# Optimization experiments

Measured on AMD Instinct MI355X. Metric: run time of the kernel, lower is better.

The kernel has to match this reference:

```python
import jax, jax.numpy as jnp
import numpy as np

HEADS = 6
WIN = 7
SHIFT = 3
NEG = -100.0


def _rel_index():
    # Swin relative position index, [49, 49] int
    coords = np.stack(np.meshgrid(np.arange(WIN), np.arange(WIN), indexing='ij')).reshape(2, -1)
    rel = (coords[:, :, None] - coords[:, None, :]).transpose(1, 2, 0)
    rel[:, :, 0] += WIN - 1
    rel[:, :, 1] += WIN - 1
    rel[:, :, 0] *= 2 * WIN - 1
    return rel.sum(-1)


def _shift_mask(H, W):
    # additive shift mask per window, [num_windows, 49, 49]
    img = np.zeros([H, W])
    slices = (slice(0, -WIN), slice(-WIN, -SHIFT), slice(-SHIFT, None))
    cnt = 0
    for h in slices:
        for w in slices:
            img[h, w] = cnt
            cnt += 1
    mw = img.reshape(H // WIN, WIN, W // WIN, WIN).transpose(0, 2, 1, 3).reshape(-1, WIN * WIN)
    diff = mw[:, None, :] - mw[:, :, None]
    return np.where(diff != 0, NEG, 0.0).astype(np.float32)


def setup_inputs() -> dict:
    key = jax.random.key(0)
    ks = jax.random.split(key, 6)
    B, H, W, C = 64, 56, 56, 192
    return {
        'x': jax.random.normal(ks[0], (B, H, W, C), jnp.float32),
        'qkv_w': jax.random.normal(ks[1], (C, 3 * C), jnp.float32) * 0.02,
        'qkv_b': jax.random.normal(ks[2], (3 * C,), jnp.float32) * 0.02,
        'rel_table': jax.random.normal(ks[3], ((2 * WIN - 1) ** 2, HEADS), jnp.float32) * 0.02,
        'proj_w': jax.random.normal(ks[4], (C, C), jnp.float32) * 0.02,
        'proj_b': jax.random.normal(ks[5], (C,), jnp.float32) * 0.02,
    }


def reference(x, qkv_w, qkv_b, rel_table, proj_w, proj_b):
    B, H, W, C = x.shape
    hd = C // HEADS
    scale = hd ** -0.5
    mask = jnp.asarray(_shift_mask(H, W))            # [nW, N, N]
    idx = _rel_index().reshape(-1)                   # static numpy [N*N]

    # cyclic shift + window partition
    xs = jnp.roll(x, (-SHIFT, -SHIFT), (1, 2))
    xw = xs.reshape(B, H // WIN, WIN, W // WIN, WIN, C)
    xw = xw.transpose(0, 1, 3, 2, 4, 5).reshape(-1, WIN * WIN, C)  # [Bn, N, C]
    Bn, N, _ = xw.shape

    qkv = (xw @ qkv_w + qkv_b).reshape(Bn, N, 3, HEADS, hd).transpose(2, 0, 3, 1, 4)
    q, k, v = qkv[0] * scale, qkv[1], qkv[2]         # [Bn, h, N, hd]

    attn = jax.nn.softmax(jnp.einsum('bhnd,bhmd->bhnm', q, k), axis=-1)

    # NOTE: original module adds relative bias and shift mask AFTER softmax
    bias = rel_table[idx].reshape(N, N, HEADS).transpose(2, 0, 1)  # [h, N, N]
    attn = attn + bias[None]
    nW = mask.shape[0]
    attn = (attn.reshape(Bn // nW, nW, HEADS, N, N) + mask[None, :, None]).reshape(Bn, HEADS, N, N)

    out = jnp.einsum('bhnm,bhmd->bhnd', attn, v).transpose(0, 2, 1, 3).reshape(Bn, N, C)
    out = out @ proj_w + proj_b

    # window reverse + un-shift
    out = out.reshape(B, H // WIN, W // WIN, WIN, WIN, C)
    out = out.transpose(0, 1, 3, 2, 4, 5).reshape(B, H, W, C)
    return jnp.roll(out, (SHIFT, SHIFT), (1, 2))
```

## Files before the change

kernel.cpp:

```cpp
#include <hip/hip_runtime.h>
#include <hip/hip_bf16.h>

typedef __attribute__((ext_vector_type(8))) short bf16x8_t;
typedef __attribute__((ext_vector_type(4))) float f32x4_t;

#define MFMA16 __builtin_amdgcn_mfma_f32_16x16x32_bf16

__device__ __forceinline__ unsigned short f2bf(float f) {
    return __builtin_bit_cast(unsigned short, __float2bfloat16(f));
}
__device__ __forceinline__ int cvt_pk_bf16(float lo, float hi) {
    int r;
    asm("v_cvt_pk_bf16_f32 %0, %1, %2" : "=v"(r) : "v"(lo), "v"(hi));
    return r;
}

__device__ __forceinline__ void group_barrier(int* cnt, int target, int ln) {
    asm volatile("s_waitcnt lgkmcnt(0)" ::: "memory");
    if (ln == 0)
        __hip_atomic_fetch_add(cnt, 1, __ATOMIC_RELEASE, __HIP_MEMORY_SCOPE_WORKGROUP);
    while (__hip_atomic_load(cnt, __ATOMIC_ACQUIRE, __HIP_MEMORY_SCOPE_WORKGROUP) < target)
        __builtin_amdgcn_s_sleep(1);
    __builtin_amdgcn_sched_barrier(0);
}

#define GRP_STRIDE 49152
#define ROWOFF_OFF 98304
#define BAR_OFF    98816
#define SMEM_BYTES 98832

__device__ __forceinline__ int qk_byte(int row, int d) {
    return row * 64 + ((((d >> 3) ^ ((row >> 1) & 3)) << 4) | ((d & 7) << 1));
}
__device__ __forceinline__ int vt_byte(int d, int tok) {
    return d * 128 + ((((tok >> 3) ^ (d & 7)) << 4) | ((tok & 7) << 1));
}

__global__ void prep_weights(const float* __restrict__ qkv_w, const float* __restrict__ proj_w,
                             unsigned short* __restrict__ wqkvT, unsigned short* __restrict__ wprojT)
{
    int i = blockIdx.x * 256 + threadIdx.x;
    if (i < 576 * 192) {
        int n = i / 192, k = i - n * 192;
        wqkvT[i] = f2bf(qkv_w[k * 576 + n]);
    }
    if (i < 192 * 192) {
        int n = i / 192, k = i - n * 192;
        wprojT[i] = f2bf(proj_w[k * 192 + n]);
    }
}

__global__ void prep_bias(const float* __restrict__ rel_table, float* __restrict__ biasT)
{
    int i = blockIdx.x * 256 + threadIdx.x;
    if (i >= 4 * 6 * 16 * 64) return;
    int ln  = i & 63;
    int f   = (i >> 6) & 15;
    int h   = (i >> 10) % 6;
    int wt  = i / 6144;
    int l15 = ln & 15, lg = ln >> 4;
    int mk  = f >> 2, nq = f & 3;
    int qt  = nq * 16 + l15;
    bool bh = (wt & 2) != 0, bw = (wt & 1) != 0;
    float4 o = {0.f, 0.f, 0.f, 0.f};
    float* po = (float*)&o;
    int iq = qt / 7, jq = qt - iq * 7;
    int regq = (bh ? ((iq < 4) ? 3 : 6) : 0) + (bw ? ((jq < 4) ? 1 : 2) : 0);
    for (int r = 0; r < 4; ++r) {
        int kt = mk * 16 + lg * 4 + r;
        if (kt < 49 && qt < 49) {
            int ik = kt / 7, jk = kt - ik * 7;
            int idx = (iq - ik + 6) * 13 + (jq - jk + 6);
            int regk = (bh ? ((ik < 4) ? 3 : 6) : 0) + (bw ? ((jk < 4) ? 1 : 2) : 0);
            po[r] = rel_table[idx * 6 + h] + ((regk != regq) ? -100.0f : 0.0f);
        }
    }
    ((float4*)biasT)[i] = o;
}

__global__ __launch_bounds__(768, 3)
void swin_fused(const float* __restrict__ x,
                const float* __restrict__ qkv_b,
                const float* __restrict__ proj_b,
                const unsigned short* __restrict__ wqkvT,
                const unsigned short* __restrict__ wprojT,
                const float* __restrict__ biasT,
                float* __restrict__ out)
{
    __shared__ unsigned char smem[SMEM_BYTES];

    const int tid = threadIdx.x;
    const int wv  = tid >> 6;
    const int g   = (wv >= 6) ? 1 : 0;
    const int h   = wv - 6 * g;
    const int ln  = tid & 63;
    const int l15 = ln & 15;
    const int lg  = ln >> 4;
    const int tg  = tid - g * 384;

    const int bw  = blockIdx.x * 2 + g;
    const int b   = bw >> 6;
    const int win = bw & 63;
    const int wh  = win >> 3;
    const int ww  = win & 7;
    const int wt  = ((wh == 7) ? 2 : 0) | ((ww == 7) ? 1 : 0);

    const unsigned gbase = g * GRP_STRIDE;
    const unsigned hbase = gbase + h * 8192;
    int* rowOff = (int*)(smem + ROWOFF_OFF + g * 256);
    int* bar    = (int*)(smem + BAR_OFF) + g;
    const f32x4_t zero4 = {0.f, 0.f, 0.f, 0.f};

    if (tid < 2) ((int*)(smem + BAR_OFF))[tid] = 0;
    __syncthreads();

#pragma unroll
    for (int it = 0; it < 8; ++it) {
        int idx = tg + it * 384;
        int n   = idx / 48;
        int c4  = idx - n * 48;
        int2* dst = (int2*)(smem + gbase + n * 400 + c4 * 8);
        if (n < 49) {
            int i = n / 7, j = n - i * 7;
            int sh = wh * 7 + i + 3; if (sh >= 56) sh -= 56;
            int sw = ww * 7 + j + 3; if (sw >= 56) sw -= 56;
            int ro = ((b * 56 + sh) * 56 + sw) * 192;
            if (c4 == 0) rowOff[n] = ro;
            const float4* src = (const float4*)(x + ro + c4 * 4);
            float4 v = *src;
            int2 p;
            p.x = cvt_pk_bf16(v.x, v.y);
            p.y = cvt_pk_bf16(v.z, v.w);
            *dst = p;
        } else {
            *dst = make_int2(0, 0);
        }
    }
    group_barrier(bar, 6, ln);

    f32x4_t accq[4][6];
#pragma unroll
    for (int mt = 0; mt < 4; ++mt)
#pragma unroll
        for (int nt = 0; nt < 6; ++nt) accq[mt][nt] = zero4;
#pragma unroll
    for (int ks = 0; ks < 6; ++ks) {
        bf16x8_t af[4];
#pragma unroll
        for (int mt = 0; mt < 4; ++mt)
            af[mt] = *(const bf16x8_t*)(smem + gbase + (mt * 16 + l15) * 400 + (ks * 32 + lg * 8) * 2);
        bf16x8_t bfv[6];
#pragma unroll
        for (int nt = 0; nt < 6; ++nt)
            bfv[nt] = *(const bf16x8_t*)(wqkvT + ((nt >> 1) * 192 + h * 32 + (nt & 1) * 16 + l15) * 192 + ks * 32 + lg * 8);
        __builtin_amdgcn_s_setprio(1);
#pragma unroll
        for (int nt = 0; nt < 6; ++nt)
#pragma unroll
            for (int mt = 0; mt < 4; ++mt)
                accq[mt][nt] = MFMA16(af[mt], bfv[nt], accq[mt][nt], 0, 0, 0);
        __builtin_amdgcn_s_setprio(0);
    }
    int vbf[4][2][2];
#pragma unroll
    for (int nv = 0; nv < 2; ++nv) {
        float bb = qkv_b[384 + h * 32 + nv * 16 + l15];
#pragma unroll
        for (int mt = 0; mt < 4; ++mt) {
            vbf[mt][nv][0] = cvt_pk_bf16(accq[mt][4 + nv][0] + bb, accq[mt][4 + nv][1] + bb);
            vbf[mt][nv][1] = cvt_pk_bf16(accq[mt][4 + nv][2] + bb, accq[mt][4 + nv][3] + bb);
        }
    }
    group_barrier(bar, 12, ln);

#pragma unroll
    for (int nt = 0; nt < 4; ++nt) {
        int part = nt >> 1;
        int d    = (nt & 1) * 16 + l15;
        float bb = qkv_b[part * 192 + h * 32 + d];
        unsigned base = hbase + part * 4096;
#pragma unroll
        for (int mt = 0; mt < 4; ++mt)
#pragma unroll
            for (int r = 0; r < 4; ++r) {
                int row = mt * 16 + lg * 4 + r;
                *(unsigned short*)(smem + base + qk_byte(row, d)) = f2bf(accq[mt][nt][r] + bb);
            }
    }
    __builtin_amdgcn_sched_barrier(0);

    f32x4_t s[4][4];
    {
        bf16x8_t kf[4], qf[4];
#pragma unroll
        for (int mk = 0; mk < 4; ++mk) {
            int row = mk * 16 + l15;
            kf[mk] = *(const bf16x8_t*)(smem + hbase + 4096 + row * 64 + ((lg ^ ((row >> 1) & 3)) << 4));
        }
#pragma unroll
        for (int nq = 0; nq < 4; ++nq) {
            int row = nq * 16 + l15;
            qf[nq] = *(const bf16x8_t*)(smem + hbase + row * 64 + ((lg ^ ((row >> 1) & 3)) << 4));
        }
        __builtin_amdgcn_s_setprio(1);
#pragma unroll
        for (int mk = 0; mk < 4; ++mk)
#pragma unroll
            for (int nq = 0; nq < 4; ++nq)
                s[mk][nq] = MFMA16(kf[mk], qf[nq], zero4, 0, 0, 0);
        __builtin_amdgcn_s_setprio(0);
    }
    __builtin_amdgcn_sched_barrier(0);

#pragma unroll
    for (int nv = 0; nv < 2; ++nv) {
        int d = nv * 16 + l15;
#pragma unroll
        for (int mt = 0; mt < 4; ++mt) {
            int tok = mt * 16 + lg * 4;
            *(int2*)(smem + hbase + vt_byte(d, tok)) = make_int2(vbf[mt][nv][0], vbf[mt][nv][1]);
        }
    }

    float4 bv4[4][4];
    {
        const float4* bp = (const float4*)biasT + (wt * 6 + h) * 16 * 64 + ln;
#pragma unroll
        for (int mk = 0; mk < 4; ++mk)
#pragma unroll
            for (int nq = 0; nq < 4; ++nq)
                bv4[mk][nq] = bp[(mk * 4 + nq) * 64];
    }

    const float C = 0.17677669529663687f * 1.4426950408889634f;
#pragma unroll
    for (int nq = 0; nq < 4; ++nq) {
        float sum = 0.f;
#pragma unroll
        for (int mk = 0; mk < 4; ++mk)
#pragma unroll
            for (int r = 0; r < 4; ++r) {
                int kt = mk * 16 + lg * 4 + r;
                float e = (kt < 49) ? __builtin_amdgcn_exp2f(C * s[mk][nq][r]) : 0.0f;
                s[mk][nq][r] = e;
                sum += e;
            }
        sum += __shfl_xor(sum, 16);
        sum += __shfl_xor(sum, 32);
        float inv = __builtin_amdgcn_rcpf(sum);
#pragma unroll
        for (int mk = 0; mk < 4; ++mk)
#pragma unroll
            for (int r = 0; r < 4; ++r) s[mk][nq][r] *= inv;
    }

#pragma unroll
    for (int mk = 0; mk < 4; ++mk)
#pragma unroll
        for (int nq = 0; nq < 4; ++nq) {
            s[mk][nq][0] += bv4[mk][nq].x;
            s[mk][nq][1] += bv4[mk][nq].y;
            s[mk][nq][2] += bv4[mk][nq].z;
            s[mk][nq][3] += bv4[mk][nq].w;
        }

    int w[4][4][2];
#pragma unroll
    for (int mk = 0; mk < 4; ++mk)
#pragma unroll
        for (int nq = 0; nq < 4; ++nq) {
            w[mk][nq][0] = cvt_pk_bf16(s[mk][nq][0], s[mk][nq][1]);
            w[mk][nq][1] = cvt_pk_bf16(s[mk][nq][2], s[mk][nq][3]);
        }

    f32x4_t o[2][4];
#pragma unroll
    for (int md = 0; md < 2; ++md)
#pragma unroll
        for (int nq = 0; nq < 4; ++nq) o[md][nq] = zero4;

    const unsigned Abase = hbase + 4096;
#pragma unroll
    for (int ks = 0; ks < 2; ++ks) {
#pragma unroll
        for (int mh = 0; mh < 2; ++mh) {
            int mk = ks * 2 + mh;
            int d  = mh * 16 + lg * 4;
#pragma unroll
            for (int nq = 0; nq < 4; ++nq) {
                int qt = nq * 16 + l15;
                *(int2*)(smem + Abase + qk_byte(qt, d)) = make_int2(w[mk][nq][0], w[mk][nq][1]);
            }
        }
        __builtin_amdgcn_sched_barrier(0);
        bf16x8_t vf[2], bfr[4];
#pragma unroll
        for (int md = 0; md < 2; ++md) {
            int d = md * 16 + l15;
            vf[md] = *(const bf16x8_t*)(smem + hbase + d * 128 + (((ks * 4 + lg) ^ (d & 7)) << 4));
        }
#pragma unroll
        for (int nq = 0; nq < 4; ++nq) {
            int qt = nq * 16 + l15;
            bfr[nq] = *(const bf16x8_t*)(smem + Abase + qt * 64 + ((lg ^ ((qt >> 1) & 3)) << 4));
        }
        __builtin_amdgcn_s_setprio(1);
#pragma unroll
        for (int nq = 0; nq < 4; ++nq)
#pragma unroll
            for (int md = 0; md < 2; ++md)
                o[md][nq] = MFMA16(vf[md], bfr[nq], o[md][nq], 0, 0, 0);
        __builtin_amdgcn_s_setprio(0);
        __builtin_amdgcn_sched_barrier(0);
    }
    group_barrier(bar, 18, ln);

#pragma unroll
    for (int md = 0; md < 2; ++md)
#pragma unroll
        for (int nq = 0; nq < 4; ++nq) {
            int qt = nq * 16 + l15;
            int ch = h * 32 + md * 16 + lg * 4;
            int d0 = cvt_pk_bf16(o[md][nq][0], o[md][nq][1]);
            int d1 = cvt_pk_bf16(o[md][nq][2], o[md][nq][3]);
            *(int2*)(smem + gbase + qt * 400 + ch * 2) = make_int2(d0, d1);
        }
    group_barrier(bar, 24, ln);

    f32x4_t y[4][2];
#pragma unroll
    for (int mt = 0; mt < 4; ++mt) { y[mt][0] = zero4; y[mt][1] = zero4; }
#pragma unroll
    for (int ks = 0; ks < 6; ++ks) {
        bf16x8_t aa[4], bb[2];
#pragma unroll
        for (int mt = 0; mt < 4; ++mt)
            aa[mt] = *(const bf16x8_t*)(smem + gbase + (mt * 16 + l15) * 400 + (ks * 32 + lg * 8) * 2);
#pragma unroll
        for (int nt = 0; nt < 2; ++nt)
            bb[nt] = *(const bf16x8_t*)(wprojT + (h * 32 + nt * 16 + l15) * 192 + ks * 32 + lg * 8);
        __builtin_amdgcn_s_setprio(1);
#pragma unroll
        for (int mt = 0; mt < 4; ++mt)
#pragma unroll
            for (int nt = 0; nt < 2; ++nt)
                y[mt][nt] = MFMA16(aa[mt], bb[nt], y[mt][nt], 0, 0, 0);
        __builtin_amdgcn_s_setprio(0);
    }
    float pb0 = proj_b[h * 32 + l15];
    float pb1 = proj_b[h * 32 + 16 + l15];
#pragma unroll
    for (int mt = 0; mt < 4; ++mt)
#pragma unroll
        for (int r = 0; r < 4; ++r) {
            int row = mt * 16 + lg * 4 + r;
            if (row < 49) {
                int ro = rowOff[row];
                out[ro + h * 32 + l15]      = y[mt][0][r] + pb0;
                out[ro + h * 32 + 16 + l15] = y[mt][1][r] + pb1;
            }
        }
}

extern "C" void kernel_launch(void* const* d_in, const int* in_sizes, int n_in,
                              void* d_out, int out_size, void* d_ws, size_t ws_size,
                              hipStream_t stream) {
    const float* x         = (const float*)d_in[0];
    const float* qkv_w     = (const float*)d_in[1];
    const float* qkv_b     = (const float*)d_in[2];
    const float* rel_table = (const float*)d_in[3];
    const float* proj_w    = (const float*)d_in[4];
    const float* proj_b    = (const float*)d_in[5];
    float* out = (float*)d_out;

    unsigned short* wqkvT  = (unsigned short*)d_ws;
    unsigned short* wprojT = wqkvT + 576 * 192;
    float* biasT = (float*)((char*)d_ws + 294912);

    prep_weights<<<576, 256, 0, stream>>>(qkv_w, proj_w, wqkvT, wprojT);
    prep_bias<<<96, 256, 0, stream>>>(rel_table, biasT);
    swin_fused<<<2048, 768, 0, stream>>>(x, qkv_b, proj_b, wqkvT, wprojT, biasT, out);
}
```

Before: 232.1 us.

## Use one window per block with hardware barriers instead of group spin barriers

```diff
diff --git a/kernel.cpp b/kernel.cpp
--- a/kernel.cpp
+++ b/kernel.cpp
@@ -15,19 +15,8 @@
     return r;
 }
 
-__device__ __forceinline__ void group_barrier(int* cnt, int target, int ln) {
-    asm volatile("s_waitcnt lgkmcnt(0)" ::: "memory");
-    if (ln == 0)
-        __hip_atomic_fetch_add(cnt, 1, __ATOMIC_RELEASE, __HIP_MEMORY_SCOPE_WORKGROUP);
-    while (__hip_atomic_load(cnt, __ATOMIC_ACQUIRE, __HIP_MEMORY_SCOPE_WORKGROUP) < target)
-        __builtin_amdgcn_s_sleep(1);
-    __builtin_amdgcn_sched_barrier(0);
-}
-
-#define GRP_STRIDE 49152
-#define ROWOFF_OFF 98304
-#define BAR_OFF    98816
-#define SMEM_BYTES 98832
+#define ROWOFF_OFF 49152
+#define SMEM_BYTES 49408
 
 __device__ __forceinline__ int qk_byte(int row, int d) {
     return row * 64 + ((((d >> 3) ^ ((row >> 1) & 3)) << 4) | ((d & 7) << 1));
@@ -78,7 +67,7 @@
     ((float4*)biasT)[i] = o;
 }
 
-__global__ __launch_bounds__(768, 3)
+__global__ __launch_bounds__(384, 4)
 void swin_fused(const float* __restrict__ x,
                 const float* __restrict__ qkv_b,
                 const float* __restrict__ proj_b,
@@ -90,36 +79,28 @@
     __shared__ unsigned char smem[SMEM_BYTES];
 
     const int tid = threadIdx.x;
-    const int wv  = tid >> 6;
-    const int g   = (wv >= 6) ? 1 : 0;
-    const int h   = wv - 6 * g;
+    const int h   = tid >> 6;
     const int ln  = tid & 63;
     const int l15 = ln & 15;
     const int lg  = ln >> 4;
-    const int tg  = tid - g * 384;
-
-    const int bw  = blockIdx.x * 2 + g;
+
+    const int bw  = blockIdx.x;
     const int b   = bw >> 6;
     const int win = bw & 63;
     const int wh  = win >> 3;
     const int ww  = win & 7;
     const int wt  = ((wh == 7) ? 2 : 0) | ((ww == 7) ? 1 : 0);
 
-    const unsigned gbase = g * GRP_STRIDE;
-    const unsigned hbase = gbase + h * 8192;
-    int* rowOff = (int*)(smem + ROWOFF_OFF + g * 256);
-    int* bar    = (int*)(smem + BAR_OFF) + g;
+    const unsigned hbase = h * 8192;
+    int* rowOff = (int*)(smem + ROWOFF_OFF);
     const f32x4_t zero4 = {0.f, 0.f, 0.f, 0.f};
 
-    if (tid < 2) ((int*)(smem + BAR_OFF))[tid] = 0;
-    __syncthreads();
-
 #pragma unroll
     for (int it = 0; it < 8; ++it) {
-        int idx = tg + it * 384;
+        int idx = tid + it * 384;
         int n   = idx / 48;
         int c4  = idx - n * 48;
-        int2* dst = (int2*)(smem + gbase + n * 400 + c4 * 8);
+        int2* dst = (int2*)(smem + n * 400 + c4 * 8);
         if (n < 49) {
             int i = n / 7, j = n - i * 7;
             int sh = wh * 7 + i + 3; if (sh >= 56) sh -= 56;
@@ -136,7 +117,7 @@
             *dst = make_int2(0, 0);
         }
     }
-    group_barrier(bar, 6, ln);
+    __syncthreads();
 
     f32x4_t accq[4][6];
 #pragma unroll
@@ -148,7 +129,7 @@
         bf16x8_t af[4];
 #pragma unroll
         for (int mt = 0; mt < 4; ++mt)
-            af[mt] = *(const bf16x8_t*)(smem + gbase + (mt * 16 + l15) * 400 + (ks * 32 + lg * 8) * 2);
+            af[mt] = *(const bf16x8_t*)(smem + (mt * 16 + l15) * 400 + (ks * 32 + lg * 8) * 2);
         bf16x8_t bfv[6];
 #pragma unroll
         for (int nt = 0; nt < 6; ++nt)
@@ -171,7 +152,7 @@
             vbf[mt][nv][1] = cvt_pk_bf16(accq[mt][4 + nv][2] + bb, accq[mt][4 + nv][3] + bb);
         }
     }
-    group_barrier(bar, 12, ln);
+    __syncthreads();
 
 #pragma unroll
     for (int nt = 0; nt < 4; ++nt) {
@@ -313,7 +294,7 @@
         __builtin_amdgcn_s_setprio(0);
         __builtin_amdgcn_sched_barrier(0);
     }
-    group_barrier(bar, 18, ln);
+    __syncthreads();
 
 #pragma unroll
     for (int md = 0; md < 2; ++md)
@@ -323,9 +304,9 @@
             int ch = h * 32 + md * 16 + lg * 4;
             int d0 = cvt_pk_bf16(o[md][nq][0], o[md][nq][1]);
             int d1 = cvt_pk_bf16(o[md][nq][2], o[md][nq][3]);
-            *(int2*)(smem + gbase + qt * 400 + ch * 2) = make_int2(d0, d1);
-        }
-    group_barrier(bar, 24, ln);
+            *(int2*)(smem + qt * 400 + ch * 2) = make_int2(d0, d1);
+        }
+    __syncthreads();
 
     f32x4_t y[4][2];
 #pragma unroll
@@ -335,7 +316,7 @@
         bf16x8_t aa[4], bb[2];
 #pragma unroll
         for (int mt = 0; mt < 4; ++mt)
-            aa[mt] = *(const bf16x8_t*)(smem + gbase + (mt * 16 + l15) * 400 + (ks * 32 + lg * 8) * 2);
+            aa[mt] = *(const bf16x8_t*)(smem + (mt * 16 + l15) * 400 + (ks * 32 + lg * 8) * 2);
 #pragma unroll
         for (int nt = 0; nt < 2; ++nt)
             bb[nt] = *(const bf16x8_t*)(wprojT + (h * 32 + nt * 16 + l15) * 192 + ks * 32 + lg * 8);
@@ -379,5 +360,5 @@
 
     prep_weights<<<576, 256, 0, stream>>>(qkv_w, proj_w, wqkvT, wprojT);
     prep_bias<<<96, 256, 0, stream>>>(rel_table, biasT);
-    swin_fused<<<2048, 768, 0, stream>>>(x, qkv_b, proj_b, wqkvT, wprojT, biasT, out);
-}
+    swin_fused<<<4096, 384, 0, stream>>>(x, qkv_b, proj_b, wqkvT, wprojT, biasT, out);
+}
```

Result: slower. 489.5 us (+110.9%).

## Feed softmax weights directly to K16 MFMA, skipping the LDS round-trip

Applied to the files above, without the earlier changes.

```diff
diff --git a/kernel.cpp b/kernel.cpp
--- a/kernel.cpp
+++ b/kernel.cpp
@@ -2,9 +2,17 @@
 #include <hip/hip_bf16.h>
 
 typedef __attribute__((ext_vector_type(8))) short bf16x8_t;
+typedef __attribute__((ext_vector_type(4))) short bf16x4_t;
 typedef __attribute__((ext_vector_type(4))) float f32x4_t;
 
 #define MFMA16 __builtin_amdgcn_mfma_f32_16x16x32_bf16
+
+#if __has_builtin(__builtin_amdgcn_mfma_f32_16x16x16bf16_1k)
+#define HAVE_MFMA_K16 1
+#define MFMA16K16 __builtin_amdgcn_mfma_f32_16x16x16bf16_1k
+#else
+#define HAVE_MFMA_K16 0
+#endif
 
 __device__ __forceinline__ unsigned short f2bf(float f) {
     return __builtin_bit_cast(unsigned short, __float2bfloat16(f));
@@ -233,6 +241,7 @@
     }
 
     const float C = 0.17677669529663687f * 1.4426950408889634f;
+    int w[4][4][2];
 #pragma unroll
     for (int nq = 0; nq < 4; ++nq) {
         float sum = 0.f;
@@ -249,36 +258,42 @@
         sum += __shfl_xor(sum, 32);
         float inv = __builtin_amdgcn_rcpf(sum);
 #pragma unroll
-        for (int mk = 0; mk < 4; ++mk)
-#pragma unroll
-            for (int r = 0; r < 4; ++r) s[mk][nq][r] *= inv;
-    }
-
-#pragma unroll
-    for (int mk = 0; mk < 4; ++mk)
+        for (int mk = 0; mk < 4; ++mk) {
+            float v0 = fmaf(s[mk][nq][0], inv, bv4[mk][nq].x);
+            float v1 = fmaf(s[mk][nq][1], inv, bv4[mk][nq].y);
+            float v2 = fmaf(s[mk][nq][2], inv, bv4[mk][nq].z);
+            float v3 = fmaf(s[mk][nq][3], inv, bv4[mk][nq].w);
+            w[mk][nq][0] = cvt_pk_bf16(v0, v1);
+            w[mk][nq][1] = cvt_pk_bf16(v2, v3);
+        }
+    }
+
+    f32x4_t o[2][4];
+#pragma unroll
+    for (int md = 0; md < 2; ++md)
+#pragma unroll
+        for (int nq = 0; nq < 4; ++nq) o[md][nq] = zero4;
+
+#if HAVE_MFMA_K16
+#pragma unroll
+    for (int mk = 0; mk < 4; ++mk) {
+        bf16x4_t vt2[2];
+#pragma unroll
+        for (int md = 0; md < 2; ++md) {
+            int d = md * 16 + l15;
+            vt2[md] = *(const bf16x4_t*)(smem + hbase + vt_byte(d, mk * 16 + lg * 4));
+        }
+        __builtin_amdgcn_s_setprio(1);
 #pragma unroll
         for (int nq = 0; nq < 4; ++nq) {
-            s[mk][nq][0] += bv4[mk][nq].x;
-            s[mk][nq][1] += bv4[mk][nq].y;
-            s[mk][nq][2] += bv4[mk][nq].z;
-            s[mk][nq][3] += bv4[mk][nq].w;
-        }
-
-    int w[4][4][2];
-#pragma unroll
-    for (int mk = 0; mk < 4; ++mk)
-#pragma unroll
-        for (int nq = 0; nq < 4; ++nq) {
-            w[mk][nq][0] = cvt_pk_bf16(s[mk][nq][0], s[mk][nq][1]);
-            w[mk][nq][1] = cvt_pk_bf16(s[mk][nq][2], s[mk][nq][3]);
-        }
-
-    f32x4_t o[2][4];
-#pragma unroll
-    for (int md = 0; md < 2; ++md)
-#pragma unroll
-        for (int nq = 0; nq < 4; ++nq) o[md][nq] = zero4;
-
+            bf16x4_t wb = __builtin_bit_cast(bf16x4_t, make_int2(w[mk][nq][0], w[mk][nq][1]));
+#pragma unroll
+            for (int md = 0; md < 2; ++md)
+                o[md][nq] = MFMA16K16(vt2[md], wb, o[md][nq], 0, 0, 0);
+        }
+        __builtin_amdgcn_s_setprio(0);
+    }
+#else
     const unsigned Abase = hbase + 4096;
 #pragma unroll
     for (int ks = 0; ks < 2; ++ks) {
@@ -313,6 +328,7 @@
         __builtin_amdgcn_s_setprio(0);
         __builtin_amdgcn_sched_barrier(0);
     }
+#endif
     group_barrier(bar, 18, ln);
 
 #pragma unroll
```

New measurement: 231.5 us. Within noise of the previous version (-0.3%).
